# Kernel tuning notes

Hardware: AMD Instinct MI355X
Metric: run time of the kernel (lower is better)

The kernel has to match this reference:

```python
import jax, jax.numpy as jnp
import numpy as np

DM, NHEAD = 1024, 16
DK = DM // NHEAD
B, S = 4, 2048


def setup_inputs() -> dict:
    key = jax.random.key(0)
    ks = jax.random.split(key, 9)
    sc = 0.02
    return {
        "q": jax.random.normal(ks[0], (B, S, DM), jnp.float32),
        "k": jax.random.normal(ks[1], (B, S, DM), jnp.float32),
        "v": jax.random.normal(ks[2], (B, S, DM), jnp.float32),
        "mask": jax.random.randint(ks[3], (B, 1, S, S), 0, 2, jnp.int32),
        "Wq": jax.random.normal(ks[4], (DM, DM), jnp.float32) * sc,
        "Wk": jax.random.normal(ks[5], (DM, DM), jnp.float32) * sc,
        "Wv": jax.random.normal(ks[6], (DM, DM), jnp.float32) * sc,
        "Wo": jax.random.normal(ks[7], (DM, DM), jnp.float32) * sc,
        "bo": jax.random.normal(ks[8], (DM,), jnp.float32) * sc,
    }


def reference(q, k, v, mask, Wq, Wk, Wv, Wo, bo):
    Bq, Sq, _ = q.shape
    # project and split heads: [B, H, S, dk]
    def heads(x, W):
        return (x @ W.T).reshape(Bq, -1, NHEAD, DK).transpose(0, 2, 1, 3)
    qh, kh, vh = heads(q, Wq), heads(k, Wk), heads(v, Wv)
    # scaled dot-product attention, full [B,H,S,S] scores (faithful to source)
    scores = jnp.einsum("bhqd,bhkd->bhqk", qh, kh) * (1.0 / np.sqrt(DK).astype(np.float32))
    scores = jnp.where(mask == 0, jnp.float32(-1e9), scores)
    attention = jax.nn.softmax(scores, axis=-1)
    context = jnp.einsum("bhqk,bhkd->bhqd", attention, vh)
    context = context.transpose(0, 2, 1, 3).reshape(Bq, Sq, DM)
    context = context @ Wo.T + bo  # output projection (dropout is identity in eval)
    return (context, attention)
```

## Files before the change

### kernel.cpp

```cpp
#include <hip/hip_runtime.h>
#include <math.h>
#include <stdint.h>

#define B_   4
#define S_   2048
#define DM_  1024
#define H_   16
#define DK_  64

typedef __bf16 bhalf;
typedef __bf16 bhalf8 __attribute__((ext_vector_type(8)));
typedef float  f32x4  __attribute__((ext_vector_type(4)));

typedef const __attribute__((address_space(1))) void g_void;
typedef __attribute__((address_space(3))) void l_void;

__device__ __forceinline__ void gld16(const void* g, void* l) {
  __builtin_amdgcn_global_load_lds((g_void*)g, (l_void*)l, 16, 0, 0);
}

__global__ __launch_bounds__(256) void cvt_kernel(const float* __restrict__ src,
                                                  bhalf* __restrict__ dst, int n) {
  int i = (blockIdx.x * 256 + threadIdx.x) * 8;
  if (i >= n) return;
  float4 a = *(const float4*)(src + i);
  float4 b = *(const float4*)(src + i + 4);
  bhalf8 o;
  o[0] = (bhalf)a.x; o[1] = (bhalf)a.y; o[2] = (bhalf)a.z; o[3] = (bhalf)a.w;
  o[4] = (bhalf)b.x; o[5] = (bhalf)b.y; o[6] = (bhalf)b.z; o[7] = (bhalf)b.w;
  *(bhalf8*)(dst + i) = o;
}

__global__ __launch_bounds__(256) void maskpack_kernel(const int* __restrict__ mask,
                                                       unsigned long long* __restrict__ out) {
  int i = blockIdx.x * 256 + threadIdx.x;
  unsigned long long bits = __ballot(mask[i] != 0);
  if ((threadIdx.x & 63) == 0) out[i >> 6] = bits;
}

template <int MODE>
__global__ __launch_bounds__(256) void gemm_bt(const bhalf* __restrict__ A,
                                               const bhalf* __restrict__ Bm,
                                               bhalf* __restrict__ d16,
                                               float* __restrict__ d32,
                                               const float* __restrict__ bias,
                                               float scale) {
  constexpr int K = 1024;
  __shared__ __align__(16) bhalf As[128 * 64];
  __shared__ __align__(16) bhalf Bs[128 * 64];
  const int tid = threadIdx.x;
  const int lane = tid & 63;
  const int w = tid >> 6;
  const int wm = w & 1, wn = w >> 1;
  const int bm = blockIdx.y, bn = blockIdx.x;
  const bhalf* Ab = A + (long)bm * 128 * K;
  const bhalf* Bb = Bm + (long)bn * 128 * K;
  const int l15 = lane & 15, l4 = lane >> 4;
  f32x4 acc[4][4] = {};
  for (int kt = 0; kt < K / 64; ++kt) {
#pragma unroll
    for (int j = 0; j < 4; ++j) {
      int c = j * 256 + tid;
      int r = c >> 3, ko = (c & 7) * 8;
      gld16(Ab + (long)r * K + kt * 64 + ko, &As[c * 8]);
      gld16(Bb + (long)r * K + kt * 64 + ko, &Bs[c * 8]);
    }
    __syncthreads();
#pragma unroll
    for (int t = 0; t < 2; ++t) {
      bhalf8 af[4], bfr[4];
#pragma unroll
      for (int i = 0; i < 4; ++i)
        af[i] = *(const bhalf8*)&As[(wm * 64 + i * 16 + l15) * 64 + t * 32 + l4 * 8];
#pragma unroll
      for (int j = 0; j < 4; ++j)
        bfr[j] = *(const bhalf8*)&Bs[(wn * 64 + j * 16 + l15) * 64 + t * 32 + l4 * 8];
#pragma unroll
      for (int i = 0; i < 4; ++i)
#pragma unroll
        for (int j = 0; j < 4; ++j)
          acc[i][j] = __builtin_amdgcn_mfma_f32_16x16x32_bf16(af[i], bfr[j], acc[i][j], 0, 0, 0);
    }
    __syncthreads();
  }
#pragma unroll
  for (int i = 0; i < 4; ++i) {
#pragma unroll
    for (int j = 0; j < 4; ++j) {
#pragma unroll
      for (int r = 0; r < 4; ++r) {
        int gm = bm * 128 + wm * 64 + i * 16 + l4 * 4 + r;
        int gn = bn * 128 + wn * 64 + j * 16 + l15;
        float v = acc[i][j][r];
        if (MODE == 0) {
          int b = gm >> 11, s = gm & 2047, h = gn >> 6, d = gn & 63;
          d16[((long)(b * H_ + h) * S_ + s) * DK_ + d] = (bhalf)(v * scale);
        } else if (MODE == 1) {
          int b = gm >> 11, s = gm & 2047, h = gn >> 6, d = gn & 63;
          d16[((long)(b * H_ + h) * DK_ + d) * S_ + s] = (bhalf)v;
        } else {
          d32[(long)gm * 1024 + gn] = v + bias[gn];
        }
      }
    }
  }
}

__device__ __forceinline__ void stage_k(const char* Kg, bhalf* dst, int tid) {
#pragma unroll
  for (int j = 0; j < 4; ++j) {
    int c = j * 256 + tid, r = c >> 3, ko = (c & 7) * 16;
    gld16(Kg + r * 128 + (ko ^ ((r & 7) << 4)), (char*)dst + c * 16);
  }
}
__device__ __forceinline__ void stage_v(const char* Vg, bhalf* dst, int tid) {
#pragma unroll
  for (int j = 0; j < 4; ++j) {
    int c = j * 256 + tid, d = c >> 4, so = (c & 15) * 16;
    gld16(Vg + (long)d * (S_ * 2) + (so ^ ((d & 15) << 4)), (char*)dst + c * 16);
  }
}

__global__ __launch_bounds__(256, 2) void attn_kernel(const bhalf* __restrict__ Qh,
                                                      const bhalf* __restrict__ Kh,
                                                      const bhalf* __restrict__ Vt,
                                                      const unsigned long long* __restrict__ mb,
                                                      bhalf* __restrict__ ctx,
                                                      float* __restrict__ att) {
  __shared__ __align__(16) bhalf Kbuf[2][128 * 64];
  __shared__ __align__(16) bhalf Vs[64 * 128];
  __shared__ __align__(16) bhalf Ps[128 * 128];
  float* rsum = (float*)Vs;

  const int tid = threadIdx.x, lane = tid & 63, w = tid >> 6;
  const int wm = w & 1, wn = w >> 1;
  const int l15 = lane & 15, l4 = lane >> 4;
  const int bid = blockIdx.x;
  const int qt = bid & 15;
  const int bh = bid >> 4;
  const int b = bh >> 4;
  const long qkBase = (long)bh * S_ * DK_;
  const bhalf* Kbase = Kh + qkBase;
  const char*  Vbase = (const char*)(Vt + qkBase);
  const int lrow0 = wm * 64 + l4 * 4;
  const long mrowbase = ((long)b * S_ + qt * 128 + lrow0) * 32 + wn;

  if (tid < 128) rsum[tid] = 0.f;

  {
    const bhalf* Qg = Qh + qkBase + (long)qt * 128 * DK_;
#pragma unroll
    for (int j = 0; j < 4; ++j) { int c = j * 256 + tid; gld16(Qg + c * 8, (char*)Ps + c * 16); }
  }
  stage_k((const char*)Kbase, Kbuf[0], tid);
  asm volatile("s_waitcnt vmcnt(4) lgkmcnt(0)" ::: "memory");
  __builtin_amdgcn_s_barrier();

  bhalf8 qf[4][2];
#pragma unroll
  for (int i = 0; i < 4; ++i)
#pragma unroll
    for (int t = 0; t < 2; ++t)
      qf[i][t] = *(const bhalf8*)((const char*)Ps + (wm * 64 + i * 16 + l15) * 128 + t * 64 + l4 * 16);

  unsigned long long mw[4][4];
#pragma unroll
  for (int i = 0; i < 4; ++i)
#pragma unroll
    for (int r = 0; r < 4; ++r) mw[i][r] = mb[mrowbase + (i * 16 + r) * 32];

  float psum[4][4] = {};
#pragma unroll 1
  for (int kt = 0; kt < 16; ++kt) {
    if (kt < 15) {
      stage_k((const char*)(Kbase + (kt + 1) * 128 * DK_), Kbuf[(kt + 1) & 1], tid);
      asm volatile("s_waitcnt vmcnt(4)" ::: "memory");
    } else {
      asm volatile("s_waitcnt vmcnt(0)" ::: "memory");
    }
    __builtin_amdgcn_s_barrier();
    const bhalf* Kc = Kbuf[kt & 1];
#pragma unroll
    for (int i = 0; i < 4; ++i) {
      unsigned int mlo[4], mhi[4];
#pragma unroll
      for (int r = 0; r < 4; ++r) {
        unsigned long long sh = mw[i][r] >> l15;
        mlo[r] = (unsigned int)sh; mhi[r] = (unsigned int)(sh >> 32);
      }
#pragma unroll
      for (int jn = 0; jn < 4; ++jn) {
        const int kr = wn * 64 + jn * 16 + l15;
        bhalf8 bk0 = *(const bhalf8*)((const char*)Kc + ((kr * 128 + l4 * 16) ^ ((kr & 7) << 4)));
        bhalf8 bk1 = *(const bhalf8*)((const char*)Kc + ((kr * 128 + 64 + l4 * 16) ^ ((kr & 7) << 4)));
        f32x4 sacc = {};
        sacc = __builtin_amdgcn_mfma_f32_16x16x32_bf16(qf[i][0], bk0, sacc, 0, 0, 0);
        sacc = __builtin_amdgcn_mfma_f32_16x16x32_bf16(qf[i][1], bk1, sacc, 0, 0, 0);
#pragma unroll
        for (int r = 0; r < 4; ++r) {
          unsigned int on = (jn < 2 ? mlo[r] : mhi[r]) & (1u << ((jn & 1) * 16));
          psum[i][r] += on ? __builtin_amdgcn_exp2f(sacc[r]) : 0.f;
        }
      }
    }
    if (kt < 15) {
#pragma unroll
      for (int i = 0; i < 4; ++i)
#pragma unroll
        for (int r = 0; r < 4; ++r) mw[i][r] = mb[mrowbase + (i * 16 + r) * 32 + (kt + 1) * 2];
    }
    __builtin_amdgcn_s_barrier();
  }

#pragma unroll
  for (int i = 0; i < 4; ++i)
#pragma unroll
    for (int r = 0; r < 4; ++r) {
      float v = psum[i][r];
      v += __shfl_xor(v, 1); v += __shfl_xor(v, 2);
      v += __shfl_xor(v, 4); v += __shfl_xor(v, 8);
      if (l15 == 0) atomicAdd(&rsum[lrow0 + i * 16 + r], v);
    }
  __syncthreads();
  if (tid < 128) rsum[tid] = -__log2f(rsum[tid]);
  __syncthreads();
  float l2r[4][4];
#pragma unroll
  for (int i = 0; i < 4; ++i)
#pragma unroll
    for (int r = 0; r < 4; ++r) l2r[i][r] = rsum[lrow0 + i * 16 + r];
  __syncthreads();

  stage_k((const char*)Kbase, Kbuf[0], tid);
#pragma unroll
  for (int i = 0; i < 4; ++i)
#pragma unroll
    for (int r = 0; r < 4; ++r) mw[i][r] = mb[mrowbase + (i * 16 + r) * 32];
  stage_v(Vbase, Vs, tid);

  f32x4 oacc[2][4] = {};
  const int prow = w * 32;
#pragma unroll 1
  for (int kt = 0; kt < 16; ++kt) {
    const int cur = kt & 1;
    if (kt < 15) {
      stage_k((const char*)(Kbase + (kt + 1) * 128 * DK_), Kbuf[cur ^ 1], tid);
      asm volatile("s_waitcnt vmcnt(8)" ::: "memory");
    } else {
      asm volatile("s_waitcnt vmcnt(4)" ::: "memory");
    }
    __builtin_amdgcn_s_barrier();
    const bhalf* Kc = Kbuf[cur];
#pragma unroll
    for (int i = 0; i < 4; ++i) {
      f32x4 cin;
      unsigned int mlo[4], mhi[4];
#pragma unroll
      for (int r = 0; r < 4; ++r) {
        cin[r] = l2r[i][r];
        unsigned long long sh = mw[i][r] >> l15;
        mlo[r] = (unsigned int)sh; mhi[r] = (unsigned int)(sh >> 32);
      }
#pragma unroll
      for (int jn = 0; jn < 4; ++jn) {
        const int kr = wn * 64 + jn * 16 + l15;
        bhalf8 bk0 = *(const bhalf8*)((const char*)Kc + ((kr * 128 + l4 * 16) ^ ((kr & 7) << 4)));
        bhalf8 bk1 = *(const bhalf8*)((const char*)Kc + ((kr * 128 + 64 + l4 * 16) ^ ((kr & 7) << 4)));
        f32x4 sacc = cin;
        sacc = __builtin_amdgcn_mfma_f32_16x16x32_bf16(qf[i][0], bk0, sacc, 0, 0, 0);
        sacc = __builtin_amdgcn_mfma_f32_16x16x32_bf16(qf[i][1], bk1, sacc, 0, 0, 0);
        const int pc2 = (wn * 64 + jn * 16 + l15) * 2;
#pragma unroll
        for (int r = 0; r < 4; ++r) {
          unsigned int on = (jn < 2 ? mlo[r] : mhi[r]) & (1u << ((jn & 1) * 16));
          float p = on ? __builtin_amdgcn_exp2f(sacc[r]) : 0.f;
          const int pr = lrow0 + i * 16 + r;
          *(bhalf*)((char*)Ps + pr * 256 + (pc2 ^ ((pr & 15) << 4))) = (bhalf)p;
        }
      }
    }
    if (kt < 15) asm volatile("s_waitcnt vmcnt(4) lgkmcnt(0)" ::: "memory");
    else         asm volatile("s_waitcnt vmcnt(0) lgkmcnt(0)" ::: "memory");
    __builtin_amdgcn_s_barrier();
    {
      float* dst = att + ((long)bh * S_ + qt * 128) * S_ + kt * 128;
#pragma unroll
      for (int rep = 0; rep < 8; ++rep) {
        int idx = rep * 256 + tid;
        int row = idx >> 4, slot = idx & 15;
        bhalf8 p8 = *(const bhalf8*)((const char*)Ps + row * 256 + ((slot * 16) ^ ((row & 15) << 4)));
        f32x4 o0, o1;
        o0[0] = (float)p8[0]; o0[1] = (float)p8[1]; o0[2] = (float)p8[2]; o0[3] = (float)p8[3];
        o1[0] = (float)p8[4]; o1[1] = (float)p8[5]; o1[2] = (float)p8[6]; o1[3] = (float)p8[7];
        float* dp = dst + (long)row * S_ + slot * 8;
        __builtin_nontemporal_store(o0, (f32x4*)dp);
        __builtin_nontemporal_store(o1, (f32x4*)(dp + 4));
      }
    }
    __builtin_amdgcn_s_setprio(1);
#pragma unroll
    for (int t = 0; t < 4; ++t) {
      bhalf8 ap[2], bv[4];
#pragma unroll
      for (int mi = 0; mi < 2; ++mi) {
        const int pr = prow + mi * 16 + l15;
        ap[mi] = *(const bhalf8*)((const char*)Ps + pr * 256 + ((t * 64 + l4 * 16) ^ ((pr & 15) << 4)));
      }
#pragma unroll
      for (int nj = 0; nj < 4; ++nj) {
        const int vr = nj * 16 + l15;
        bv[nj] = *(const bhalf8*)((const char*)Vs + vr * 256 + ((t * 64 + l4 * 16) ^ ((vr & 15) << 4)));
      }
#pragma unroll
      for (int mi = 0; mi < 2; ++mi)
#pragma unroll
        for (int nj = 0; nj < 4; ++nj)
          oacc[mi][nj] = __builtin_amdgcn_mfma_f32_16x16x32_bf16(ap[mi], bv[nj], oacc[mi][nj], 0, 0, 0);
    }
    __builtin_amdgcn_s_setprio(0);
    __builtin_amdgcn_s_barrier();
    if (kt < 15) {
#pragma unroll
      for (int i = 0; i < 4; ++i)
#pragma unroll
        for (int r = 0; r < 4; ++r) mw[i][r] = mb[mrowbase + (i * 16 + r) * 32 + (kt + 1) * 2];
      stage_v(Vbase + (kt + 1) * 256, Vs, tid);
    }
  }
#pragma unroll
  for (int mi = 0; mi < 2; ++mi)
#pragma unroll
    for (int nj = 0; nj < 4; ++nj)
#pragma unroll
      for (int r = 0; r < 4; ++r) {
        int lq = prow + mi * 16 + l4 * 4 + r;
        int d = nj * 16 + l15;
        int gq = qt * 128 + lq;
        ctx[((long)(b * S_ + gq)) * DM_ + (bh & 15) * DK_ + d] = (bhalf)oacc[mi][nj][r];
      }
}

extern "C" void kernel_launch(void* const* d_in, const int* in_sizes, int n_in,
                              void* d_out, int out_size, void* d_ws, size_t ws_size,
                              hipStream_t stream) {
  const float* q  = (const float*)d_in[0];
  const float* k  = (const float*)d_in[1];
  const float* v  = (const float*)d_in[2];
  const int*   mask = (const int*)d_in[3];
  const float* Wq = (const float*)d_in[4];
  const float* Wk = (const float*)d_in[5];
  const float* Wv = (const float*)d_in[6];
  const float* Wo = (const float*)d_in[7];
  const float* bo = (const float*)d_in[8];
  float* out = (float*)d_out;
  float* att = out + (size_t)B_ * S_ * DM_;

  char* ws = (char*)d_ws;
  bhalf* qb  = (bhalf*)(ws);
  bhalf* kb  = (bhalf*)(ws + (16ull << 20));
  bhalf* vb  = (bhalf*)(ws + (32ull << 20));
  bhalf* Wqb = (bhalf*)(ws + (48ull << 20));
  bhalf* Wkb = (bhalf*)(ws + (50ull << 20));
  bhalf* Wvb = (bhalf*)(ws + (52ull << 20));
  bhalf* Wob = (bhalf*)(ws + (54ull << 20));
  bhalf* Qh  = (bhalf*)(ws + (56ull << 20));
  bhalf* Kh  = (bhalf*)(ws + (72ull << 20));
  bhalf* Vt  = (bhalf*)(ws + (88ull << 20));
  bhalf* ctx = (bhalf*)(ws + (104ull << 20));
  unsigned long long* mb = (unsigned long long*)(ws + (120ull << 20));

  const int NQKV = B_ * S_ * DM_;
  const int NW = DM_ * DM_;
  cvt_kernel<<<NQKV / 2048, 256, 0, stream>>>(q, qb, NQKV);
  cvt_kernel<<<NQKV / 2048, 256, 0, stream>>>(k, kb, NQKV);
  cvt_kernel<<<NQKV / 2048, 256, 0, stream>>>(v, vb, NQKV);
  cvt_kernel<<<NW / 2048, 256, 0, stream>>>(Wq, Wqb, NW);
  cvt_kernel<<<NW / 2048, 256, 0, stream>>>(Wk, Wkb, NW);
  cvt_kernel<<<NW / 2048, 256, 0, stream>>>(Wv, Wvb, NW);
  cvt_kernel<<<NW / 2048, 256, 0, stream>>>(Wo, Wob, NW);
  maskpack_kernel<<<(B_ * S_ * S_) / 256, 256, 0, stream>>>(mask, mb);

  dim3 gg(DM_ / 128, (B_ * S_) / 128);
  gemm_bt<0><<<gg, 256, 0, stream>>>(qb, Wqb, Qh, nullptr, nullptr, 0.18033688011112042f);
  gemm_bt<0><<<gg, 256, 0, stream>>>(kb, Wkb, Kh, nullptr, nullptr, 1.0f);
  gemm_bt<1><<<gg, 256, 0, stream>>>(vb, Wvb, Vt, nullptr, nullptr, 1.0f);

  attn_kernel<<<B_ * H_ * (S_ / 128), 256, 0, stream>>>(Qh, Kh, Vt, mb, ctx, att);

  gemm_bt<2><<<gg, 256, 0, stream>>>(ctx, Wob, nullptr, out, bo, 1.0f);
}
```

Baseline: 1.573 ms.

## Batch conversion launches, remap GEMM workgroups, relax attention load waits

```diff
diff --git a/kernel.cpp b/kernel.cpp
--- a/kernel.cpp
+++ b/kernel.cpp
@@ -19,16 +19,31 @@
   __builtin_amdgcn_global_load_lds((g_void*)g, (l_void*)l, 16, 0, 0);
 }
 
-__global__ __launch_bounds__(256) void cvt_kernel(const float* __restrict__ src,
-                                                  bhalf* __restrict__ dst, int n) {
+__device__ __forceinline__ void cvt_body(const float* __restrict__ s, bhalf* __restrict__ d) {
   int i = (blockIdx.x * 256 + threadIdx.x) * 8;
-  if (i >= n) return;
-  float4 a = *(const float4*)(src + i);
-  float4 b = *(const float4*)(src + i + 4);
+  float4 a = *(const float4*)(s + i);
+  float4 b = *(const float4*)(s + i + 4);
   bhalf8 o;
   o[0] = (bhalf)a.x; o[1] = (bhalf)a.y; o[2] = (bhalf)a.z; o[3] = (bhalf)a.w;
   o[4] = (bhalf)b.x; o[5] = (bhalf)b.y; o[6] = (bhalf)b.z; o[7] = (bhalf)b.w;
-  *(bhalf8*)(dst + i) = o;
+  *(bhalf8*)(d + i) = o;
+}
+
+__global__ __launch_bounds__(256) void cvt3_kernel(const float* __restrict__ s0, const float* __restrict__ s1,
+                                                   const float* __restrict__ s2, bhalf* __restrict__ d0,
+                                                   bhalf* __restrict__ d1, bhalf* __restrict__ d2) {
+  const float* s = blockIdx.y == 0 ? s0 : blockIdx.y == 1 ? s1 : s2;
+  bhalf* d = blockIdx.y == 0 ? d0 : blockIdx.y == 1 ? d1 : d2;
+  cvt_body(s, d);
+}
+
+__global__ __launch_bounds__(256) void cvt4_kernel(const float* __restrict__ s0, const float* __restrict__ s1,
+                                                   const float* __restrict__ s2, const float* __restrict__ s3,
+                                                   bhalf* __restrict__ d0, bhalf* __restrict__ d1,
+                                                   bhalf* __restrict__ d2, bhalf* __restrict__ d3) {
+  const float* s = blockIdx.y == 0 ? s0 : blockIdx.y == 1 ? s1 : blockIdx.y == 2 ? s2 : s3;
+  bhalf* d = blockIdx.y == 0 ? d0 : blockIdx.y == 1 ? d1 : blockIdx.y == 2 ? d2 : d3;
+  cvt_body(s, d);
 }
 
 __global__ __launch_bounds__(256) void maskpack_kernel(const int* __restrict__ mask,
@@ -52,7 +67,10 @@
   const int lane = tid & 63;
   const int w = tid >> 6;
   const int wm = w & 1, wn = w >> 1;
-  const int bm = blockIdx.y, bn = blockIdx.x;
+  const int flat = blockIdx.y * gridDim.x + blockIdx.x;
+  const int nwg = gridDim.x * gridDim.y;
+  const int wg = (flat & 7) * (nwg >> 3) + (flat >> 3);
+  const int bm = wg >> 3, bn = wg & 7;
   const bhalf* Ab = A + (long)bm * 128 * K;
   const bhalf* Bb = Bm + (long)bn * 128 * K;
   const int l15 = lane & 15, l4 = lane >> 4;
@@ -168,15 +186,16 @@
   for (int i = 0; i < 4; ++i)
 #pragma unroll
     for (int r = 0; r < 4; ++r) mw[i][r] = mb[mrowbase + (i * 16 + r) * 32];
+  asm volatile("s_waitcnt vmcnt(20)" ::: "memory");
 
   float psum[4][4] = {};
 #pragma unroll 1
   for (int kt = 0; kt < 16; ++kt) {
     if (kt < 15) {
       stage_k((const char*)(Kbase + (kt + 1) * 128 * DK_), Kbuf[(kt + 1) & 1], tid);
-      asm volatile("s_waitcnt vmcnt(4)" ::: "memory");
+      asm volatile("s_waitcnt vmcnt(20)" ::: "memory");
     } else {
-      asm volatile("s_waitcnt vmcnt(0)" ::: "memory");
+      asm volatile("s_waitcnt vmcnt(16)" ::: "memory");
     }
     __builtin_amdgcn_s_barrier();
     const bhalf* Kc = Kbuf[kt & 1];
@@ -208,6 +227,7 @@
       for (int i = 0; i < 4; ++i)
 #pragma unroll
         for (int r = 0; r < 4; ++r) mw[i][r] = mb[mrowbase + (i * 16 + r) * 32 + (kt + 1) * 2];
+      asm volatile("s_waitcnt vmcnt(20)" ::: "memory");
     }
     __builtin_amdgcn_s_barrier();
   }
@@ -236,6 +256,7 @@
   for (int i = 0; i < 4; ++i)
 #pragma unroll
     for (int r = 0; r < 4; ++r) mw[i][r] = mb[mrowbase + (i * 16 + r) * 32];
+  asm volatile("s_waitcnt vmcnt(20)" ::: "memory");
   stage_v(Vbase, Vs, tid);
 
   f32x4 oacc[2][4] = {};
@@ -243,11 +264,14 @@
 #pragma unroll 1
   for (int kt = 0; kt < 16; ++kt) {
     const int cur = kt & 1;
-    if (kt < 15) {
+    if (kt == 0) {
+      stage_k((const char*)(Kbase + 128 * DK_), Kbuf[1], tid);
+      asm volatile("s_waitcnt vmcnt(8)" ::: "memory");
+    } else if (kt < 15) {
       stage_k((const char*)(Kbase + (kt + 1) * 128 * DK_), Kbuf[cur ^ 1], tid);
-      asm volatile("s_waitcnt vmcnt(8)" ::: "memory");
+      asm volatile("s_waitcnt vmcnt(40)" ::: "memory");
     } else {
-      asm volatile("s_waitcnt vmcnt(4)" ::: "memory");
+      asm volatile("s_waitcnt vmcnt(36)" ::: "memory");
     }
     __builtin_amdgcn_s_barrier();
     const bhalf* Kc = Kbuf[cur];
@@ -282,6 +306,13 @@
     if (kt < 15) asm volatile("s_waitcnt vmcnt(4) lgkmcnt(0)" ::: "memory");
     else         asm volatile("s_waitcnt vmcnt(0) lgkmcnt(0)" ::: "memory");
     __builtin_amdgcn_s_barrier();
+    if (kt < 15) {
+#pragma unroll
+      for (int i = 0; i < 4; ++i)
+#pragma unroll
+        for (int r = 0; r < 4; ++r) mw[i][r] = mb[mrowbase + (i * 16 + r) * 32 + (kt + 1) * 2];
+      asm volatile("s_waitcnt vmcnt(20)" ::: "memory");
+    }
     {
       float* dst = att + ((long)bh * S_ + qt * 128) * S_ + kt * 128;
 #pragma unroll
@@ -320,11 +351,8 @@
     __builtin_amdgcn_s_setprio(0);
     __builtin_amdgcn_s_barrier();
     if (kt < 15) {
-#pragma unroll
-      for (int i = 0; i < 4; ++i)
-#pragma unroll
-        for (int r = 0; r < 4; ++r) mw[i][r] = mb[mrowbase + (i * 16 + r) * 32 + (kt + 1) * 2];
       stage_v(Vbase + (kt + 1) * 256, Vs, tid);
+      asm volatile("s_waitcnt vmcnt(40)" ::: "memory");
     }
   }
 #pragma unroll
@@ -371,13 +399,10 @@
 
   const int NQKV = B_ * S_ * DM_;
   const int NW = DM_ * DM_;
-  cvt_kernel<<<NQKV / 2048, 256, 0, stream>>>(q, qb, NQKV);
-  cvt_kernel<<<NQKV / 2048, 256, 0, stream>>>(k, kb, NQKV);
-  cvt_kernel<<<NQKV / 2048, 256, 0, stream>>>(v, vb, NQKV);
-  cvt_kernel<<<NW / 2048, 256, 0, stream>>>(Wq, Wqb, NW);
-  cvt_kernel<<<NW / 2048, 256, 0, stream>>>(Wk, Wkb, NW);
-  cvt_kernel<<<NW / 2048, 256, 0, stream>>>(Wv, Wvb, NW);
-  cvt_kernel<<<NW / 2048, 256, 0, stream>>>(Wo, Wob, NW);
+  dim3 g3(NQKV / 2048, 3);
+  cvt3_kernel<<<g3, 256, 0, stream>>>(q, k, v, qb, kb, vb);
+  dim3 g4(NW / 2048, 4);
+  cvt4_kernel<<<g4, 256, 0, stream>>>(Wq, Wk, Wv, Wo, Wqb, Wkb, Wvb, Wob);
   maskpack_kernel<<<(B_ * S_ * S_) / 256, 256, 0, stream>>>(mask, mb);
 
   dim3 gg(DM_ / 128, (B_ * S_) / 128);
```

After: 1.570 ms. Within noise of the previous version (-0.2%).
